# Optimization experiments

Measured on AMD Instinct MI355X. Metric: run time of the kernel, lower is better.

Reference implementation:

```python
import jax, jax.numpy as jnp
import numpy as np

EPS = 1e-8
LN_EPS = 1e-5

def _layernorm(x, g, b):
    mu = jnp.mean(x, axis=-1, keepdims=True)
    var = jnp.mean((x - mu) ** 2, axis=-1, keepdims=True)
    return (x - mu) / jnp.sqrt(var + LN_EPS) * g + b

def setup_inputs() -> dict:
    key = jax.random.key(0)
    ks = jax.random.split(key, 10)
    B, S = 8192, 4096
    input_dim, hidden_dim = 4, 256
    h4 = hidden_dim // 4  # 64
    price_series = jax.random.uniform(ks[0], (B, S, 1), dtype=jnp.float32) + 0.5
    # 4 parallel encoders stacked on leading axis: Linear(input_dim->h4) + LayerNorm(h4)
    enc_w = jax.random.normal(ks[1], (4, input_dim, h4), dtype=jnp.float32) * 0.5
    enc_b = jax.random.normal(ks[2], (4, h4), dtype=jnp.float32) * 0.02
    enc_g = jnp.ones((4, h4), dtype=jnp.float32)
    enc_beta = jnp.zeros((4, h4), dtype=jnp.float32)
    # regime head: Linear(hidden_dim->64) + ReLU + (Dropout eval=identity) + Linear(64->4)
    head_w1 = jax.random.normal(ks[3], (hidden_dim, 64), dtype=jnp.float32) * 0.0625
    head_b1 = jnp.zeros((64,), dtype=jnp.float32)
    head_w2 = jax.random.normal(ks[4], (64, 4), dtype=jnp.float32) * 0.125
    head_b2 = jnp.zeros((4,), dtype=jnp.float32)
    return {"price_series": price_series, "enc_w": enc_w, "enc_b": enc_b,
            "enc_g": enc_g, "enc_beta": enc_beta,
            "head_w1": head_w1, "head_b1": head_b1,
            "head_w2": head_w2, "head_b2": head_b2}

def reference(price_series, enc_w, enc_b, enc_g, enc_beta, head_w1, head_b1, head_w2, head_b2):
    prices = price_series[:, :, 0]  # [B, S]
    B, S = prices.shape
    # Rolling SMA(20) with clamped window start, via cumsum (single pass, no per-step loop)
    csum = jnp.concatenate([jnp.zeros((B, 1), prices.dtype), jnp.cumsum(prices, axis=1)], axis=1)  # [B, S+1]
    i = jnp.arange(S)
    start20 = jnp.maximum(0, i - 19)
    cnt20 = (i - start20 + 1).astype(prices.dtype)
    sma20 = (csum[:, i + 1] - csum[:, start20]) / cnt20  # [B, S]
    trend_signal = (prices - sma20) / (sma20 + EPS)
    f_trend = jnp.mean(trend_signal, axis=1, keepdims=True)  # [B,1]
    # momentum over last 10 steps
    p_last = prices[:, -1:]
    p_m10 = prices[:, -10:-9]
    f_mom = (p_last - p_m10) / (p_m10 + EPS)  # [B,1]
    # mean reversion
    p_mean = jnp.mean(prices, axis=1, keepdims=True)
    f_mr = (p_last - p_mean) / (p_mean + EPS)  # [B,1]
    # cycle: coefficient of variation (torch.std is unbiased, ddof=1)
    f_cyc = jnp.std(prices, axis=1, ddof=1, keepdims=True) / (p_mean + EPS)  # [B,1]
    combined = jnp.concatenate([f_trend, f_mom, f_mr, f_cyc], axis=1)  # [B, 4]
    # 4 parallel encoders: Linear -> ReLU -> LayerNorm
    pre = jnp.einsum('bi,eio->ebo', combined, enc_w) + enc_b[:, None, :]  # [4, B, 64]
    feats = _layernorm(jax.nn.relu(pre), enc_g[:, None, :], enc_beta[:, None, :])  # [4, B, 64]
    # concat order: trend, momentum, mean_rev, cycle along feature dim
    regime_features = jnp.transpose(feats, (1, 0, 2)).reshape(B, -1)  # [B, 256]
    h = jax.nn.relu(regime_features @ head_w1 + head_b1)
    regime_probs = jax.nn.softmax(h @ head_w2 + head_b2, axis=1)  # [B, 4]
    return (regime_features, regime_probs)
```

## Files before the change

### kernel.cpp

```cpp
#include <hip/hip_runtime.h>

#define EPS 1e-8f
#define LN_EPS 1e-5f
#define NROWS 8192
#define SLEN 4096
#define PROBS_OFF 2097152

typedef __attribute__((ext_vector_type(8))) short bf16x8;
typedef __attribute__((ext_vector_type(4))) float f32x4;

__device__ __forceinline__ short f2bf(float f) {
    unsigned u = __float_as_uint(f);
    unsigned r = (u + 0x7FFFu + ((u >> 16) & 1u)) >> 16;
    return (short)r;
}

__device__ __forceinline__ void g2l16(const float4* g, float4* l) {
    __builtin_amdgcn_global_load_lds(
        (const __attribute__((address_space(1))) unsigned int*)g,
        (__attribute__((address_space(3))) unsigned int*)l,
        16, 0, 0);
}

__device__ __forceinline__ int swz(int s) { return s ^ ((s >> 3) & 7); }

__global__ __launch_bounds__(256) void k_feat(const float* __restrict__ prices,
                                              float* __restrict__ ws) {
    __shared__ float4 sld4[1032];
    __shared__ float red[4][3];

    const int t = threadIdx.x;
    const int b = blockIdx.x;
    const int lane = t & 63, wv = t >> 6;
    const float4* R4 = (const float4*)(prices + (size_t)b * SLEN);

    if (t < 8) sld4[t] = make_float4(0.f, 0.f, 0.f, 0.f);

    #pragma unroll
    for (int k = 0; k < 4; ++k) {
        const int base = 8 + 256 * k + 64 * wv;
        const int g = swz(base + lane) - 8;
        g2l16(R4 + g, sld4 + base);
    }
    __syncthreads();

    float4 q0 = sld4[swz(4 * t + 3)];
    float4 q1 = sld4[swz(4 * t + 4)];
    float4 q2 = sld4[swz(4 * t + 5)];
    float4 q3 = sld4[swz(4 * t + 6)];
    float4 q4 = sld4[swz(4 * t + 7)];
    float4 s0 = sld4[swz(4 * t + 8)];
    float4 s1 = sld4[swz(4 * t + 9)];
    float4 s2 = sld4[swz(4 * t + 10)];
    float4 s3 = sld4[swz(4 * t + 11)];

    float xv[16] = { s0.x, s0.y, s0.z, s0.w, s1.x, s1.y, s1.z, s1.w,
                     s2.x, s2.y, s2.z, s2.w, s3.x, s3.y, s3.z, s3.w };
    float ov[16] = { q0.x, q0.y, q0.z, q0.w, q1.x, q1.y, q1.z, q1.w,
                     q2.x, q2.y, q2.z, q2.w, q3.x, q3.y, q3.z, q3.w };

    float W = q0.y + q0.z + q0.w
            + q1.x + q1.y + q1.z + q1.w
            + q2.x + q2.y + q2.z + q2.w
            + q3.x + q3.y + q3.z + q3.w
            + q4.x + q4.y + q4.z + q4.w;

    float sum = 0.0f, sq = 0.0f, ts = 0.0f;
    if (t >= 2) {
        #pragma unroll
        for (int j = 0; j < 16; ++j) {
            float x = xv[j];
            W += (j == 0) ? x : (x - ov[j]);
            sum += x;
            sq = fmaf(x, x, sq);
            float num = fmaf(x, 20.0f, -W);
            float den = W + (20.0f * EPS);
            ts += num * __builtin_amdgcn_rcpf(den);
        }
    } else {
        const float pf = (float)(16 * t);
        #pragma unroll
        for (int j = 0; j < 16; ++j) {
            float x = xv[j];
            W += (j == 0) ? x : (x - ov[j]);
            sum += x;
            sq = fmaf(x, x, sq);
            float c = fminf(pf + (float)(j + 1), 20.0f);
            float num = fmaf(x, c, -W);
            float den = fmaf(EPS, c, W);
            ts += num * __builtin_amdgcn_rcpf(den);
        }
    }

    #pragma unroll
    for (int off = 32; off > 0; off >>= 1) {
        sum += __shfl_xor(sum, off);
        sq  += __shfl_xor(sq,  off);
        ts  += __shfl_xor(ts,  off);
    }
    if (lane == 0) { red[wv][0] = sum; red[wv][1] = sq; red[wv][2] = ts; }
    __syncthreads();

    if (t == 255) {
        float S = red[0][0] + red[1][0] + red[2][0] + red[3][0];
        float Q = red[0][1] + red[1][1] + red[2][1] + red[3][1];
        float T = red[0][2] + red[1][2] + red[2][2] + red[3][2];
        float mean = S * (1.0f / 4096.0f);
        float var  = fmaxf((Q - 4096.0f * mean * mean) * (1.0f / 4095.0f), 0.0f);
        float p_m10 = s1.z, p_last = s3.w;
        float4 f;
        f.x = T * (1.0f / 4096.0f);
        f.y = (p_last - p_m10) / (p_m10 + EPS);
        f.z = (p_last - mean) / (mean + EPS);
        f.w = sqrtf(var) / (mean + EPS);
        ((float4*)ws)[b] = f;
    }
}

#define ROWS 16

__global__ __launch_bounds__(256) void k_head(
    const float* __restrict__ ws, float* __restrict__ out,
    const float* __restrict__ enc_w, const float* __restrict__ enc_b,
    const float* __restrict__ enc_g, const float* __restrict__ enc_bt,
    const float* __restrict__ w1, const float* __restrict__ b1,
    const float* __restrict__ w2, const float* __restrict__ b2)
{
    __shared__ float comb[ROWS][4];
    __shared__ short rfb[ROWS][264];
    __shared__ float hbuf[ROWS][68];

    const int t = threadIdx.x;
    const int r0 = blockIdx.x * ROWS;
    const int lane = t & 63, wave = t >> 6;
    const int l15 = lane & 15, q = lane >> 4;

    if (t < ROWS) *(float4*)comb[t] = ((const float4*)ws)[r0 + t];

    bf16x8 bfrag[8];
    #pragma unroll
    for (int kt = 0; kt < 8; ++kt) {
        #pragma unroll
        for (int j = 0; j < 8; ++j) {
            int k = kt * 32 + q * 8 + j;
            bfrag[kt][j] = f2bf(w1[k * 64 + wave * 16 + l15]);
        }
    }

    const float ew0 = enc_w[wave * 256 + lane];
    const float ew1v = enc_w[wave * 256 + 64 + lane];
    const float ew2v = enc_w[wave * 256 + 128 + lane];
    const float ew3v = enc_w[wave * 256 + 192 + lane];
    const float ebv = enc_b[t], egv = enc_g[t], btv = enc_bt[t];

    __syncthreads();

    for (int r = 0; r < ROWS; r += 2) {
        float4 cba = *(const float4*)comb[r];
        float4 cbb = *(const float4*)comb[r + 1];
        float va = fmaf(cba.x, ew0, fmaf(cba.y, ew1v, fmaf(cba.z, ew2v, fmaf(cba.w, ew3v, ebv))));
        float vb = fmaf(cbb.x, ew0, fmaf(cbb.y, ew1v, fmaf(cbb.z, ew2v, fmaf(cbb.w, ew3v, ebv))));
        va = fmaxf(va, 0.0f);
        vb = fmaxf(vb, 0.0f);
        float sma = va, smb = vb;
        #pragma unroll
        for (int off = 32; off > 0; off >>= 1) {
            sma += __shfl_xor(sma, off);
            smb += __shfl_xor(smb, off);
        }
        float mua = sma * (1.0f / 64.0f);
        float mub = smb * (1.0f / 64.0f);
        float da = va - mua, db = vb - mub;
        float vsa = da * da, vsb = db * db;
        #pragma unroll
        for (int off = 32; off > 0; off >>= 1) {
            vsa += __shfl_xor(vsa, off);
            vsb += __shfl_xor(vsb, off);
        }
        float ya = fmaf(da * rsqrtf(vsa * (1.0f / 64.0f) + LN_EPS), egv, btv);
        float yb = fmaf(db * rsqrtf(vsb * (1.0f / 64.0f) + LN_EPS), egv, btv);
        out[(size_t)(r0 + r) * 256 + t] = ya;
        out[(size_t)(r0 + r + 1) * 256 + t] = yb;
        rfb[r][t] = f2bf(ya);
        rfb[r + 1][t] = f2bf(yb);
    }
    __syncthreads();

    f32x4 acc0 = {0.f, 0.f, 0.f, 0.f};
    #pragma unroll
    for (int kt = 0; kt < 8; ++kt) {
        bf16x8 a0 = *(const bf16x8*)&rfb[l15][kt * 32 + q * 8];
        acc0 = __builtin_amdgcn_mfma_f32_16x16x32_bf16(a0, bfrag[kt], acc0, 0, 0, 0);
    }

    const int col = wave * 16 + l15;
    const float b1v = b1[col];
    #pragma unroll
    for (int rg = 0; rg < 4; ++rg)
        hbuf[q * 4 + rg][col] = fmaxf(acc0[rg] + b1v, 0.0f);
    __syncthreads();

    if (t < 4 * ROWS) {
        int r = t >> 2, c = t & 3;
        float a0 = 0.f, a1 = 0.f, a2 = 0.f, a3 = 0.f;
        #pragma unroll
        for (int j = 0; j < 16; ++j) {
            a0 = fmaf(hbuf[r][j],      w2[j * 4 + c],        a0);
            a1 = fmaf(hbuf[r][16 + j], w2[(16 + j) * 4 + c], a1);
            a2 = fmaf(hbuf[r][32 + j], w2[(32 + j) * 4 + c], a2);
            a3 = fmaf(hbuf[r][48 + j], w2[(48 + j) * 4 + c], a3);
        }
        float lg = b2[c] + ((a0 + a1) + (a2 + a3));
        float mx = fmaxf(lg, __shfl_xor(lg, 1, 4));
        mx = fmaxf(mx, __shfl_xor(mx, 2, 4));
        float ex = __expf(lg - mx);
        float s2 = ex + __shfl_xor(ex, 1, 4);
        s2 += __shfl_xor(s2, 2, 4);
        out[PROBS_OFF + (size_t)(r0 + r) * 4 + c] = ex / s2;
    }
}

extern "C" void kernel_launch(void* const* d_in, const int* in_sizes, int n_in,
                              void* d_out, int out_size, void* d_ws, size_t ws_size,
                              hipStream_t stream) {
    const float* prices  = (const float*)d_in[0];
    const float* enc_w   = (const float*)d_in[1];
    const float* enc_b   = (const float*)d_in[2];
    const float* enc_g   = (const float*)d_in[3];
    const float* enc_bt  = (const float*)d_in[4];
    const float* head_w1 = (const float*)d_in[5];
    const float* head_b1 = (const float*)d_in[6];
    const float* head_w2 = (const float*)d_in[7];
    const float* head_b2 = (const float*)d_in[8];
    float* out = (float*)d_out;
    float* ws  = (float*)d_ws;

    k_feat<<<NROWS, 256, 0, stream>>>(prices, ws);
    k_head<<<NROWS / ROWS, 256, 0, stream>>>(ws, out, enc_w, enc_b, enc_g, enc_bt,
                                             head_w1, head_b1, head_w2, head_b2);
}
```

Baseline: 212.7 us.

## Fuse feature reduction and head into one kernel with triple-buffered row loads

Merges the per-row feature kernel and the head kernel into one kernel where each block processes 16 rows. Price rows are streamed into a 3-slot LDS ring via async global-to-LDS loads with manual waitcnt/barrier pipelining, and the features go to shared memory instead of the workspace. This removes a launch and the workspace round trip. In exchange, the grid shrinks to 512 blocks and rows are processed serially per block, which reduces memory-level parallelism.

```diff
diff --git a/kernel.cpp b/kernel.cpp
--- a/kernel.cpp
+++ b/kernel.cpp
@@ -5,6 +5,7 @@
 #define NROWS 8192
 #define SLEN 4096
 #define PROBS_OFF 2097152
+#define RPB 16
 
 typedef __attribute__((ext_vector_type(8))) short bf16x8;
 typedef __attribute__((ext_vector_type(4))) float f32x4;
@@ -24,118 +25,136 @@
 
 __device__ __forceinline__ int swz(int s) { return s ^ ((s >> 3) & 7); }
 
-__global__ __launch_bounds__(256) void k_feat(const float* __restrict__ prices,
-                                              float* __restrict__ ws) {
-    __shared__ float4 sld4[1032];
-    __shared__ float red[4][3];
-
-    const int t = threadIdx.x;
-    const int b = blockIdx.x;
-    const int lane = t & 63, wv = t >> 6;
-    const float4* R4 = (const float4*)(prices + (size_t)b * SLEN);
-
-    if (t < 8) sld4[t] = make_float4(0.f, 0.f, 0.f, 0.f);
-
-    #pragma unroll
-    for (int k = 0; k < 4; ++k) {
-        const int base = 8 + 256 * k + 64 * wv;
-        const int g = swz(base + lane) - 8;
-        g2l16(R4 + g, sld4 + base);
-    }
-    __syncthreads();
-
-    float4 q0 = sld4[swz(4 * t + 3)];
-    float4 q1 = sld4[swz(4 * t + 4)];
-    float4 q2 = sld4[swz(4 * t + 5)];
-    float4 q3 = sld4[swz(4 * t + 6)];
-    float4 q4 = sld4[swz(4 * t + 7)];
-    float4 s0 = sld4[swz(4 * t + 8)];
-    float4 s1 = sld4[swz(4 * t + 9)];
-    float4 s2 = sld4[swz(4 * t + 10)];
-    float4 s3 = sld4[swz(4 * t + 11)];
-
-    float xv[16] = { s0.x, s0.y, s0.z, s0.w, s1.x, s1.y, s1.z, s1.w,
-                     s2.x, s2.y, s2.z, s2.w, s3.x, s3.y, s3.z, s3.w };
-    float ov[16] = { q0.x, q0.y, q0.z, q0.w, q1.x, q1.y, q1.z, q1.w,
-                     q2.x, q2.y, q2.z, q2.w, q3.x, q3.y, q3.z, q3.w };
-
-    float W = q0.y + q0.z + q0.w
-            + q1.x + q1.y + q1.z + q1.w
-            + q2.x + q2.y + q2.z + q2.w
-            + q3.x + q3.y + q3.z + q3.w
-            + q4.x + q4.y + q4.z + q4.w;
-
-    float sum = 0.0f, sq = 0.0f, ts = 0.0f;
-    if (t >= 2) {
-        #pragma unroll
-        for (int j = 0; j < 16; ++j) {
-            float x = xv[j];
-            W += (j == 0) ? x : (x - ov[j]);
-            sum += x;
-            sq = fmaf(x, x, sq);
-            float num = fmaf(x, 20.0f, -W);
-            float den = W + (20.0f * EPS);
-            ts += num * __builtin_amdgcn_rcpf(den);
-        }
-    } else {
-        const float pf = (float)(16 * t);
-        #pragma unroll
-        for (int j = 0; j < 16; ++j) {
-            float x = xv[j];
-            W += (j == 0) ? x : (x - ov[j]);
-            sum += x;
-            sq = fmaf(x, x, sq);
-            float c = fminf(pf + (float)(j + 1), 20.0f);
-            float num = fmaf(x, c, -W);
-            float den = fmaf(EPS, c, W);
-            ts += num * __builtin_amdgcn_rcpf(den);
-        }
-    }
-
-    #pragma unroll
-    for (int off = 32; off > 0; off >>= 1) {
-        sum += __shfl_xor(sum, off);
-        sq  += __shfl_xor(sq,  off);
-        ts  += __shfl_xor(ts,  off);
-    }
-    if (lane == 0) { red[wv][0] = sum; red[wv][1] = sq; red[wv][2] = ts; }
-    __syncthreads();
-
-    if (t == 255) {
-        float S = red[0][0] + red[1][0] + red[2][0] + red[3][0];
-        float Q = red[0][1] + red[1][1] + red[2][1] + red[3][1];
-        float T = red[0][2] + red[1][2] + red[2][2] + red[3][2];
-        float mean = S * (1.0f / 4096.0f);
-        float var  = fmaxf((Q - 4096.0f * mean * mean) * (1.0f / 4095.0f), 0.0f);
-        float p_m10 = s1.z, p_last = s3.w;
-        float4 f;
-        f.x = T * (1.0f / 4096.0f);
-        f.y = (p_last - p_m10) / (p_m10 + EPS);
-        f.z = (p_last - mean) / (mean + EPS);
-        f.w = sqrtf(var) / (mean + EPS);
-        ((float4*)ws)[b] = f;
-    }
-}
-
-#define ROWS 16
-
-__global__ __launch_bounds__(256) void k_head(
-    const float* __restrict__ ws, float* __restrict__ out,
+__global__ __launch_bounds__(256) void k_fused(
+    const float* __restrict__ prices, float* __restrict__ out,
     const float* __restrict__ enc_w, const float* __restrict__ enc_b,
     const float* __restrict__ enc_g, const float* __restrict__ enc_bt,
     const float* __restrict__ w1, const float* __restrict__ b1,
     const float* __restrict__ w2, const float* __restrict__ b2)
 {
-    __shared__ float comb[ROWS][4];
-    __shared__ short rfb[ROWS][264];
-    __shared__ float hbuf[ROWS][68];
+    __shared__ float4 sbuf[3][1032];
+    __shared__ float red[4][3];
+    __shared__ __align__(16) float comb[RPB][4];
+    __shared__ short rfb[RPB][264];
+    __shared__ float hbuf[RPB][68];
 
     const int t = threadIdx.x;
-    const int r0 = blockIdx.x * ROWS;
-    const int lane = t & 63, wave = t >> 6;
+    const int lane = t & 63, wv = t >> 6;
+    const int r0 = blockIdx.x * RPB;
+
+    auto stage = [&](int r, int bi) {
+        const float4* R4 = (const float4*)prices + (size_t)(r0 + r) * 1024;
+        #pragma unroll
+        for (int k = 0; k < 4; ++k) {
+            const int base = 8 + 256 * k + 64 * wv;
+            const int g = swz(base + lane) - 8;
+            g2l16(R4 + g, &sbuf[bi][base]);
+        }
+    };
+
+    float pm10_l = 0.f, plast_l = 0.f;
+
+    auto compute_row = [&](int bi) {
+        float4 q0 = sbuf[bi][swz(4 * t + 3)];
+        float4 q1 = sbuf[bi][swz(4 * t + 4)];
+        float4 q2 = sbuf[bi][swz(4 * t + 5)];
+        float4 q3 = sbuf[bi][swz(4 * t + 6)];
+        float4 q4 = sbuf[bi][swz(4 * t + 7)];
+        float4 s0 = sbuf[bi][swz(4 * t + 8)];
+        float4 s1 = sbuf[bi][swz(4 * t + 9)];
+        float4 s2 = sbuf[bi][swz(4 * t + 10)];
+        float4 s3 = sbuf[bi][swz(4 * t + 11)];
+
+        float xv[16] = { s0.x, s0.y, s0.z, s0.w, s1.x, s1.y, s1.z, s1.w,
+                         s2.x, s2.y, s2.z, s2.w, s3.x, s3.y, s3.z, s3.w };
+        float ov[16] = { q0.x, q0.y, q0.z, q0.w, q1.x, q1.y, q1.z, q1.w,
+                         q2.x, q2.y, q2.z, q2.w, q3.x, q3.y, q3.z, q3.w };
+
+        float W = q0.y + q0.z + q0.w
+                + q1.x + q1.y + q1.z + q1.w
+                + q2.x + q2.y + q2.z + q2.w
+                + q3.x + q3.y + q3.z + q3.w
+                + q4.x + q4.y + q4.z + q4.w;
+
+        float sum = 0.0f, sq = 0.0f, ts = 0.0f;
+        if (t >= 2) {
+            #pragma unroll
+            for (int j = 0; j < 16; ++j) {
+                float x = xv[j];
+                W += (j == 0) ? x : (x - ov[j]);
+                sum += x;
+                sq = fmaf(x, x, sq);
+                float num = fmaf(x, 20.0f, -W);
+                float den = W + (20.0f * EPS);
+                ts += num * __builtin_amdgcn_rcpf(den);
+            }
+        } else {
+            const float pf = (float)(16 * t);
+            #pragma unroll
+            for (int j = 0; j < 16; ++j) {
+                float x = xv[j];
+                W += (j == 0) ? x : (x - ov[j]);
+                sum += x;
+                sq = fmaf(x, x, sq);
+                float c = fminf(pf + (float)(j + 1), 20.0f);
+                float num = fmaf(x, c, -W);
+                float den = fmaf(EPS, c, W);
+                ts += num * __builtin_amdgcn_rcpf(den);
+            }
+        }
+        if (t == 255) { pm10_l = s1.z; plast_l = s3.w; }
+
+        #pragma unroll
+        for (int off = 32; off > 0; off >>= 1) {
+            sum += __shfl_xor(sum, off);
+            sq  += __shfl_xor(sq,  off);
+            ts  += __shfl_xor(ts,  off);
+        }
+        if (lane == 0) { red[wv][0] = sum; red[wv][1] = sq; red[wv][2] = ts; }
+    };
+
+    auto finish_row = [&](int r) {
+        if (t == 255) {
+            float S = red[0][0] + red[1][0] + red[2][0] + red[3][0];
+            float Q = red[0][1] + red[1][1] + red[2][1] + red[3][1];
+            float T = red[0][2] + red[1][2] + red[2][2] + red[3][2];
+            float mean = S * (1.0f / 4096.0f);
+            float var  = fmaxf((Q - 4096.0f * mean * mean) * (1.0f / 4095.0f), 0.0f);
+            comb[r][0] = T * (1.0f / 4096.0f);
+            comb[r][1] = (plast_l - pm10_l) / (pm10_l + EPS);
+            comb[r][2] = (plast_l - mean) / (mean + EPS);
+            comb[r][3] = sqrtf(var) / (mean + EPS);
+        }
+    };
+
+    if (t < 8) {
+        const float4 z4 = make_float4(0.f, 0.f, 0.f, 0.f);
+        sbuf[0][t] = z4; sbuf[1][t] = z4; sbuf[2][t] = z4;
+    }
+    stage(0, 0);
+    stage(1, 1);
+
+    for (int r = 0; r < RPB - 2; ++r) {
+        stage(r + 2, (r + 2) % 3);
+        asm volatile("s_waitcnt vmcnt(8) lgkmcnt(0)\ns_barrier" ::: "memory");
+        __builtin_amdgcn_sched_barrier(0);
+        compute_row(r % 3);
+        asm volatile("s_waitcnt lgkmcnt(0)\ns_barrier" ::: "memory");
+        finish_row(r);
+    }
+    asm volatile("s_waitcnt vmcnt(4) lgkmcnt(0)\ns_barrier" ::: "memory");
+    __builtin_amdgcn_sched_barrier(0);
+    compute_row((RPB - 2) % 3);
+    asm volatile("s_waitcnt lgkmcnt(0)\ns_barrier" ::: "memory");
+    finish_row(RPB - 2);
+    asm volatile("s_waitcnt vmcnt(0) lgkmcnt(0)\ns_barrier" ::: "memory");
+    __builtin_amdgcn_sched_barrier(0);
+    compute_row((RPB - 1) % 3);
+    asm volatile("s_waitcnt lgkmcnt(0)\ns_barrier" ::: "memory");
+    finish_row(RPB - 1);
+
     const int l15 = lane & 15, q = lane >> 4;
-
-    if (t < ROWS) *(float4*)comb[t] = ((const float4*)ws)[r0 + t];
+    const int wave = wv;
 
     bf16x8 bfrag[8];
     #pragma unroll
@@ -146,8 +165,7 @@
             bfrag[kt][j] = f2bf(w1[k * 64 + wave * 16 + l15]);
         }
     }
-
-    const float ew0 = enc_w[wave * 256 + lane];
+    const float ew0  = enc_w[wave * 256 + lane];
     const float ew1v = enc_w[wave * 256 + 64 + lane];
     const float ew2v = enc_w[wave * 256 + 128 + lane];
     const float ew3v = enc_w[wave * 256 + 192 + lane];
@@ -155,7 +173,7 @@
 
     __syncthreads();
 
-    for (int r = 0; r < ROWS; r += 2) {
+    for (int r = 0; r < RPB; r += 2) {
         float4 cba = *(const float4*)comb[r];
         float4 cbb = *(const float4*)comb[r + 1];
         float va = fmaf(cba.x, ew0, fmaf(cba.y, ew1v, fmaf(cba.z, ew2v, fmaf(cba.w, ew3v, ebv))));
@@ -200,7 +218,7 @@
         hbuf[q * 4 + rg][col] = fmaxf(acc0[rg] + b1v, 0.0f);
     __syncthreads();
 
-    if (t < 4 * ROWS) {
+    if (t < 4 * RPB) {
         int r = t >> 2, c = t & 3;
         float a0 = 0.f, a1 = 0.f, a2 = 0.f, a3 = 0.f;
         #pragma unroll
@@ -233,9 +251,9 @@
     const float* head_w2 = (const float*)d_in[7];
     const float* head_b2 = (const float*)d_in[8];
     float* out = (float*)d_out;
-    float* ws  = (float*)d_ws;
-
-    k_feat<<<NROWS, 256, 0, stream>>>(prices, ws);
-    k_head<<<NROWS / ROWS, 256, 0, stream>>>(ws, out, enc_w, enc_b, enc_g, enc_bt,
-                                             head_w1, head_b1, head_w2, head_b2);
-}
+    (void)d_ws; (void)ws_size;
+
+    k_fused<<<NROWS / RPB, 256, 0, stream>>>(prices, out, enc_w, enc_b, enc_g,
+                                             enc_bt, head_w1, head_b1, head_w2,
+                                             head_b2);
+}
```

Result: no change. 214.5 us (+0.8%).
